# Optimization experiments

Hardware: AMD Instinct MI355X
Metric: run time of the kernel (lower is better)

## Reference

```python
import jax, jax.numpy as jnp
import numpy as np

N = 30000      # nodes
E = 480000     # edges (before self loops)
DIN = 128      # dim_in
DH = 32        # dim_h (per-head out channels)
H1 = 8         # gat1 heads
H2 = 2         # gat2 heads
G = 64         # num graphs in batch
DOUT = 10      # dim_out
NEG_SLOPE = 0.2


def _glorot(key, shape):
    fan_in = shape[0]
    return jax.random.normal(key, shape, dtype=jnp.float32) / np.sqrt(fan_in)


def setup_inputs() -> dict:
    key = jax.random.key(0)
    ks = jax.random.split(key, 16)
    x = jax.random.normal(ks[0], (N, DIN), dtype=jnp.float32)
    edge_index = jax.random.randint(ks[1], (2, E), 0, N, dtype=jnp.int32)
    batch = jnp.sort(jax.random.randint(ks[2], (N,), 0, G, dtype=jnp.int32))
    # GATv2Conv layer 1: lin_l, lin_r (dim_in -> H1*DH), att (H1, DH), bias (H1*DH)
    W1l = _glorot(ks[3], (DIN, H1 * DH))
    W1r = _glorot(ks[4], (DIN, H1 * DH))
    a1 = _glorot(ks[5], (DH, H1)).T  # [H1, DH]
    b1 = jnp.zeros((H1 * DH,), dtype=jnp.float32)
    # GATv2Conv layer 2: (H1*DH -> H2*DH)
    W2l = _glorot(ks[6], (H1 * DH, H2 * DH))
    W2r = _glorot(ks[7], (H1 * DH, H2 * DH))
    a2 = _glorot(ks[8], (DH, H2)).T  # [H2, DH]
    b2 = jnp.zeros((H2 * DH,), dtype=jnp.float32)
    # MLP head: fc1(2*DH -> DH), fc2(DH -> DH//2), fc(DH//2 -> DOUT); stored [in,out]
    fc1_w = _glorot(ks[9], (2 * DH, DH)); fc1_b = jnp.zeros((DH,), jnp.float32)
    fc2_w = _glorot(ks[10], (DH, DH // 2)); fc2_b = jnp.zeros((DH // 2,), jnp.float32)
    fc_w = _glorot(ks[11], (DH // 2, DOUT)); fc_b = jnp.zeros((DOUT,), jnp.float32)
    return {"x": x, "edge_index": edge_index, "batch": batch,
            "W1l": W1l, "W1r": W1r, "a1": a1, "b1": b1,
            "W2l": W2l, "W2r": W2r, "a2": a2, "b2": b2,
            "fc1_w": fc1_w, "fc1_b": fc1_b, "fc2_w": fc2_w, "fc2_b": fc2_b,
            "fc_w": fc_w, "fc_b": fc_b}


def gatv2_conv(x, edge_index, Wl, Wr, att, bias, heads, dh, n):
    """PyG GATv2Conv: concat=True, add_self_loops=True, negative_slope=0.2."""
    src, dst = edge_index[0], edge_index[1]
    loop = jnp.arange(n, dtype=src.dtype)        # self loops (PyG default)
    src = jnp.concatenate([src, loop])
    dst = jnp.concatenate([dst, loop])
    xl = (x @ Wl).reshape(n, heads, dh)          # source transform
    xr = (x @ Wr).reshape(n, heads, dh)          # destination transform
    xj = xl[src]                                  # [Etot, H, dh] message features
    s = jax.nn.leaky_relu(xj + xr[dst], NEG_SLOPE)
    e = jnp.einsum('ehd,hd->eh', s, att)          # per-edge per-head score
    # segment softmax over incoming edges of each destination node
    m = jax.ops.segment_max(e, dst, num_segments=n)
    p = jnp.exp(e - m[dst])
    z = jax.ops.segment_sum(p, dst, num_segments=n)
    alpha = p / z[dst]                            # [Etot, H]
    out = jax.ops.segment_sum(xj * alpha[..., None], dst, num_segments=n)
    return out.reshape(n, heads * dh) + bias


def reference(x, edge_index, batch, W1l, W1r, a1, b1, W2l, W2r, a2, b2,
              fc1_w, fc1_b, fc2_w, fc2_b, fc_w, fc_b):
    h = gatv2_conv(x, edge_index, W1l, W1r, a1, b1, H1, DH, N)
    h = jax.nn.elu(h)
    h = gatv2_conv(h, edge_index, W2l, W2r, a2, b2, H2, DH, N)  # [N, 2*DH]
    # global_mean_pool
    sums = jax.ops.segment_sum(h, batch, num_segments=G)
    cnt = jax.ops.segment_sum(jnp.ones((N,), h.dtype), batch, num_segments=G)
    hg = sums / jnp.maximum(cnt, 1.0)[:, None]    # [G, 2*DH]
    x1 = jax.nn.relu(hg @ fc1_w + fc1_b)
    # dropout p=0.2 is identity in eval mode
    x2 = jax.nn.relu(x1 @ fc2_w + fc2_b)
    c = x2 @ fc_w + fc_b
    return (c, x2)
```

## Files before the change

### kernel.cpp

```cpp
#include <hip/hip_runtime.h>
#include <math.h>

#define DIN 128
#define DH  32
#define H1  8
#define H2  2
#define GNUM 64
#define DOUT 10
#define NEG_SLOPE 0.2f
#define SCAN_B 512

typedef __attribute__((ext_vector_type(8))) short sv8;
typedef __attribute__((ext_vector_type(4))) short sv4;
typedef __attribute__((ext_vector_type(4))) float fv4;

static __device__ __forceinline__ unsigned short f2bf(float f) {
    unsigned int u = __float_as_uint(f);
    unsigned int r = (u + 0x7fffu + ((u >> 16) & 1u)) >> 16;
    return (unsigned short)r;
}
static __device__ __forceinline__ float bf2f(unsigned short h) {
    return __uint_as_float(((unsigned int)h) << 16);
}

__global__ void k_prep(const float* __restrict__ x,
                       const float* __restrict__ W1l, const float* __restrict__ W1r,
                       const float* __restrict__ W2l, const float* __restrict__ W2r,
                       short* __restrict__ B1th, short* __restrict__ B1tl,
                       short* __restrict__ B2th, short* __restrict__ B2tl,
                       unsigned short* __restrict__ Xh, unsigned short* __restrict__ Xl,
                       int* __restrict__ zbase, int nz, int NK) {
    int id = blockIdx.x * blockDim.x + threadIdx.x;
    if (id < nz) zbase[id] = 0;
    const int T1 = 512 * 128;
    const int T2 = 128 * 256;
    if (id < T1) {
        int n = id / 128, k = id - n * 128;
        float v = (n < 256) ? W1l[(size_t)k * 256 + n] : W1r[(size_t)k * 256 + (n - 256)];
        unsigned short h = f2bf(v);
        B1th[id] = (short)h;
        B1tl[id] = (short)f2bf(v - bf2f(h));
    } else if (id < T1 + T2) {
        int id2 = id - T1;
        int n = id2 / 256, k = id2 - n * 256;
        float v = (n < 64) ? W2l[(size_t)k * 64 + n] : W2r[(size_t)k * 64 + (n - 64)];
        unsigned short h = f2bf(v);
        B2th[id2] = (short)h;
        B2tl[id2] = (short)f2bf(v - bf2f(h));
    } else if (id < T1 + T2 + NK) {
        int e = id - T1 - T2;
        float v = x[e];
        unsigned short h = f2bf(v);
        Xh[e] = h;
        Xl[e] = f2bf(v - bf2f(h));
    }
}

__global__ void k_deg(const int* __restrict__ dst, int* __restrict__ deg, int E, int n) {
    int i = blockIdx.x * blockDim.x + threadIdx.x;
    if (i < E) {
        atomicAdd(&deg[dst[i]], 1);
    } else if (i < E + n) {
        atomicAdd(&deg[i - E], 1);
    }
}

__global__ __launch_bounds__(SCAN_B)
void k_scan_partial(const int* __restrict__ deg, int* __restrict__ bsum, int n) {
    int i = blockIdx.x * SCAN_B + threadIdx.x;
    int v = (i < n) ? deg[i] : 0;
    #pragma unroll
    for (int m = 32; m >= 1; m >>= 1) v += __shfl_xor(v, m);
    __shared__ int red[SCAN_B / 64];
    if ((threadIdx.x & 63) == 0) red[threadIdx.x >> 6] = v;
    __syncthreads();
    if (threadIdx.x == 0) {
        int s = 0;
        #pragma unroll
        for (int k = 0; k < SCAN_B / 64; ++k) s += red[k];
        bsum[blockIdx.x] = s;
    }
}

__global__ __launch_bounds__(SCAN_B)
void k_scan_apply(int* __restrict__ deg, int* __restrict__ cursor,
                  const int* __restrict__ bsum, int n, int nb) {
    __shared__ int buf[SCAN_B];
    __shared__ int pfx_s, tot_s;
    const int t = threadIdx.x, b = blockIdx.x;
    if (t < 64) {
        int v = (t < nb) ? bsum[t] : 0;
        int incl = v;
        #pragma unroll
        for (int o = 1; o < 64; o <<= 1) {
            int w = __shfl_up(incl, o);
            if (t >= o) incl += w;
        }
        int pfx = (b == 0) ? 0 : __shfl(incl, b - 1);
        int tot = __shfl(incl, nb - 1);
        if (t == 0) { pfx_s = pfx; tot_s = tot; }
    }
    int i = b * SCAN_B + t;
    int v = (i < n) ? deg[i] : 0;
    buf[t] = v;
    __syncthreads();
    for (int o = 1; o < SCAN_B; o <<= 1) {
        int a = (t >= o) ? buf[t - o] : 0;
        __syncthreads();
        buf[t] += a;
        __syncthreads();
    }
    int excl = buf[t] - v + pfx_s;
    if (i < n) { deg[i] = excl; cursor[i] = excl; }
    if (b == 0 && t == 0) deg[n] = tot_s;
}

__global__ void k_scatter(const int* __restrict__ src, const int* __restrict__ dst,
                          int* __restrict__ cursor, int* __restrict__ csr_src, int E, int n) {
    int i = blockIdx.x * blockDim.x + threadIdx.x;
    if (i < E) {
        int d = dst[i];
        int pos = atomicAdd(&cursor[d], 1);
        csr_src[pos] = src[i];
    } else if (i < E + n) {
        int v = i - E;
        int pos = atomicAdd(&cursor[v], 1);
        csr_src[pos] = v;
    }
}

__global__ __launch_bounds__(256)
void k_gemm_split(const unsigned short* __restrict__ Ah, const unsigned short* __restrict__ Al,
                  const short* __restrict__ Bth, const short* __restrict__ Btl,
                  unsigned short* __restrict__ Cl, float* __restrict__ Cr,
                  int M, int K, int Ntot, int NL) {
    __shared__ union {
        struct { short hi[128 * 40]; short lo[128 * 40]; } a;
        float c[64 * 132];
    } sm;
    const int tid = threadIdx.x;
    const int lane = tid & 63;
    const int wid = tid >> 6;
    const int wm = wid & 1, wn = wid >> 1;
    const int m0 = blockIdx.x * 128;
    const int n0 = blockIdx.y * 128;
    const int l15 = lane & 15, q = lane >> 4;

    fv4 acc[4][4] = {};

    for (int kk = 0; kk < K; kk += 32) {
        __syncthreads();
        #pragma unroll
        for (int i = 0; i < 4; ++i) {
            int idx = tid + i * 256;
            int arr = idx >> 9;
            int c = idx & 511;
            int row = c >> 2, qq = c & 3;
            int mg = m0 + row;
            const unsigned short* srcp = arr ? Al : Ah;
            sv8 v = { 0, 0, 0, 0, 0, 0, 0, 0 };
            if (mg < M) v = *(const sv8*)(srcp + (size_t)mg * K + kk + qq * 8);
            short* dst = arr ? sm.a.lo : sm.a.hi;
            *(sv8*)&dst[row * 40 + qq * 8] = v;
        }
        __syncthreads();

        sv8 bh[4], bl[4];
        #pragma unroll
        for (int fn = 0; fn < 4; ++fn) {
            int ng = n0 + wn * 64 + fn * 16 + l15;
            bh[fn] = *(const sv8*)(Bth + (size_t)ng * K + kk + q * 8);
            bl[fn] = *(const sv8*)(Btl + (size_t)ng * K + kk + q * 8);
        }
        #pragma unroll
        for (int fm = 0; fm < 4; ++fm) {
            int rl = wm * 64 + fm * 16 + l15;
            sv8 ah = *(const sv8*)&sm.a.hi[rl * 40 + q * 8];
            sv8 al = *(const sv8*)&sm.a.lo[rl * 40 + q * 8];
            #pragma unroll
            for (int fn = 0; fn < 4; ++fn) {
                acc[fm][fn] = __builtin_amdgcn_mfma_f32_16x16x32_bf16(ah, bh[fn], acc[fm][fn], 0, 0, 0);
                acc[fm][fn] = __builtin_amdgcn_mfma_f32_16x16x32_bf16(ah, bl[fn], acc[fm][fn], 0, 0, 0);
                acc[fm][fn] = __builtin_amdgcn_mfma_f32_16x16x32_bf16(al, bh[fn], acc[fm][fn], 0, 0, 0);
            }
        }
    }

    const int NR = Ntot - NL;
    #pragma unroll
    for (int s = 0; s < 2; ++s) {
        __syncthreads();
        if (wm == s) {
            #pragma unroll
            for (int fm = 0; fm < 4; ++fm)
                #pragma unroll
                for (int fn = 0; fn < 4; ++fn)
                    #pragma unroll
                    for (int r = 0; r < 4; ++r)
                        sm.c[(fm * 16 + q * 4 + r) * 132 + wn * 64 + fn * 16 + l15] = acc[fm][fn][r];
        }
        __syncthreads();
        #pragma unroll
        for (int i = 0; i < 2; ++i) {
            int lr = (tid >> 3) + i * 32;
            int grow = m0 + s * 64 + lr;
            if (grow < M) {
                #pragma unroll
                for (int k4 = 0; k4 < 4; ++k4) {
                    int jj = (tid & 7) + k4 * 8;
                    float4 vv = *(float4*)&sm.c[lr * 132 + jj * 4];
                    int gcol = n0 + jj * 4;
                    if (gcol < NL) {
                        ushort4 uu;
                        uu.x = f2bf(vv.x); uu.y = f2bf(vv.y);
                        uu.z = f2bf(vv.z); uu.w = f2bf(vv.w);
                        *(ushort4*)(Cl + (size_t)grow * NL + gcol) = uu;
                    } else {
                        *(float4*)(Cr + (size_t)grow * NR + (gcol - NL)) = vv;
                    }
                }
            }
        }
    }
}

__global__ __launch_bounds__(256)
void k_gemm_bf(const unsigned short* __restrict__ A, const short* __restrict__ Bth,
               const short* __restrict__ Btl,
               unsigned short* __restrict__ Cl, float* __restrict__ Cr,
               int M, int K, int Ntot, int NL) {
    __shared__ union {
        short a[128 * 40];
        float c[64 * 132];
    } sm;
    const int tid = threadIdx.x;
    const int lane = tid & 63;
    const int wid = tid >> 6;
    const int wm = wid & 1, wn = wid >> 1;
    const int m0 = blockIdx.x * 128;
    const int n0 = blockIdx.y * 128;
    const int l15 = lane & 15, q = lane >> 4;

    fv4 acc[4][4] = {};

    for (int kk = 0; kk < K; kk += 32) {
        __syncthreads();
        #pragma unroll
        for (int i = 0; i < 2; ++i) {
            int idx = tid + i * 256;
            int row = idx >> 2, qq = idx & 3;
            int mg = m0 + row;
            sv8 v = { 0, 0, 0, 0, 0, 0, 0, 0 };
            if (mg < M) v = *(const sv8*)(A + (size_t)mg * K + kk + qq * 8);
            *(sv8*)&sm.a[row * 40 + qq * 8] = v;
        }
        __syncthreads();

        sv8 bh[4], bl[4];
        #pragma unroll
        for (int fn = 0; fn < 4; ++fn) {
            int ng = n0 + wn * 64 + fn * 16 + l15;
            bh[fn] = *(const sv8*)(Bth + (size_t)ng * K + kk + q * 8);
            bl[fn] = *(const sv8*)(Btl + (size_t)ng * K + kk + q * 8);
        }
        #pragma unroll
        for (int fm = 0; fm < 4; ++fm) {
            int rl = wm * 64 + fm * 16 + l15;
            sv8 ah = *(const sv8*)&sm.a[rl * 40 + q * 8];
            #pragma unroll
            for (int fn = 0; fn < 4; ++fn) {
                acc[fm][fn] = __builtin_amdgcn_mfma_f32_16x16x32_bf16(ah, bh[fn], acc[fm][fn], 0, 0, 0);
                acc[fm][fn] = __builtin_amdgcn_mfma_f32_16x16x32_bf16(ah, bl[fn], acc[fm][fn], 0, 0, 0);
            }
        }
    }

    const int NR = Ntot - NL;
    #pragma unroll
    for (int s = 0; s < 2; ++s) {
        __syncthreads();
        if (wm == s) {
            #pragma unroll
            for (int fm = 0; fm < 4; ++fm)
                #pragma unroll
                for (int fn = 0; fn < 4; ++fn)
                    #pragma unroll
                    for (int r = 0; r < 4; ++r)
                        sm.c[(fm * 16 + q * 4 + r) * 132 + wn * 64 + fn * 16 + l15] = acc[fm][fn][r];
        }
        __syncthreads();
        #pragma unroll
        for (int i = 0; i < 2; ++i) {
            int lr = (tid >> 3) + i * 32;
            int grow = m0 + s * 64 + lr;
            if (grow < M) {
                #pragma unroll
                for (int k4 = 0; k4 < 4; ++k4) {
                    int jj = (tid & 7) + k4 * 8;
                    float4 vv = *(float4*)&sm.c[lr * 132 + jj * 4];
                    int gcol = n0 + jj * 4;
                    if (gcol < NL) {
                        ushort4 uu;
                        uu.x = f2bf(vv.x); uu.y = f2bf(vv.y);
                        uu.z = f2bf(vv.z); uu.w = f2bf(vv.w);
                        *(ushort4*)(Cl + (size_t)grow * NL + gcol) = uu;
                    } else {
                        *(float4*)(Cr + (size_t)grow * NR + (gcol - NL)) = vv;
                    }
                }
            }
        }
    }
}

__global__ __launch_bounds__(64)
void k_edge1(const unsigned short* __restrict__ XLB, const float* __restrict__ XR,
             const int* __restrict__ offs, const int* __restrict__ csr,
             const float* __restrict__ att, const float* __restrict__ bias,
             unsigned short* __restrict__ out, int n) {
    const int lane = threadIdx.x;
    const int v = blockIdx.x;
    const int li = lane & 31;
    const int half = lane >> 5;
    float av[8], xr[8];
    #pragma unroll
    for (int k = 0; k < 8; ++k) av[k] = att[li * 8 + k];
    #pragma unroll
    for (int k = 0; k < 8; ++k) xr[k] = XR[(size_t)v * 256 + li * 8 + k];
    const uint4* XL4 = (const uint4*)XLB;
    float z = 0.f;
    float acc[8] = {};
    const int e0 = offs[v], e1 = offs[v + 1];
    for (int j0 = e0; j0 < e1; j0 += 4) {
        #pragma unroll
        for (int p = 0; p < 2; ++p) {
            int j = j0 + p * 2 + half;
            bool valid = (j < e1);
            int jj = valid ? j : (e1 - 1);
            int src = csr[jj];
            uint4 u = XL4[(size_t)src * 32 + li];
            float f[8];
            f[0] = __uint_as_float(u.x << 16);  f[1] = __uint_as_float(u.x & 0xffff0000u);
            f[2] = __uint_as_float(u.y << 16);  f[3] = __uint_as_float(u.y & 0xffff0000u);
            f[4] = __uint_as_float(u.z << 16);  f[5] = __uint_as_float(u.z & 0xffff0000u);
            f[6] = __uint_as_float(u.w << 16);  f[7] = __uint_as_float(u.w & 0xffff0000u);
            float s1 = 0.f, s2 = 0.f;
            #pragma unroll
            for (int k = 0; k < 8; ++k) {
                float t = f[k] + xr[k];
                s1 = fmaf(t, av[k], s1);
                s2 = fmaf(fabsf(t), av[k], s2);
            }
            float s = fmaf(0.6f, s1, 0.4f * s2);
            s += __shfl_xor(s, 1);
            s += __shfl_xor(s, 2);
            float w = valid ? __expf(s) : 0.f;
            z += w;
            #pragma unroll
            for (int k = 0; k < 8; ++k) acc[k] = fmaf(w, f[k], acc[k]);
        }
    }
    z += __shfl_xor(z, 32);
    #pragma unroll
    for (int k = 0; k < 8; ++k) acc[k] += __shfl_xor(acc[k], 32);
    if (half == 0) {
        const float rz = 1.f / z;
        unsigned int o[4];
        #pragma unroll
        for (int k2 = 0; k2 < 4; ++k2) {
            float lo = fmaf(acc[k2 * 2 + 0], rz, bias[li * 8 + k2 * 2 + 0]);
            float hi = fmaf(acc[k2 * 2 + 1], rz, bias[li * 8 + k2 * 2 + 1]);
            lo = (lo > 0.f) ? lo : (__expf(lo) - 1.f);
            hi = (hi > 0.f) ? hi : (__expf(hi) - 1.f);
            o[k2] = (unsigned int)f2bf(lo) | ((unsigned int)f2bf(hi) << 16);
        }
        uint4 ov = { o[0], o[1], o[2], o[3] };
        *(uint4*)(out + (size_t)v * 256 + li * 8) = ov;
    }
}

__global__ __launch_bounds__(64)
void k_edge2(const unsigned short* __restrict__ XLB, const float* __restrict__ XR,
             const int* __restrict__ offs, const int* __restrict__ csr,
             const float* __restrict__ att, const float* __restrict__ bias,
             float* __restrict__ out, int n) {
    const int lane = threadIdx.x;
    const int v = blockIdx.x;
    const int li = lane & 7;
    const int slot = lane >> 3;
    float av[8], xr[8];
    #pragma unroll
    for (int k = 0; k < 8; ++k) av[k] = att[li * 8 + k];
    #pragma unroll
    for (int k = 0; k < 8; ++k) xr[k] = XR[(size_t)v * 64 + li * 8 + k];
    const uint4* XL4 = (const uint4*)XLB;
    float z = 0.f;
    float acc[8] = {};
    const int e0 = offs[v], e1 = offs[v + 1];
    for (int j0 = e0; j0 < e1; j0 += 8) {
        int j = j0 + slot;
        bool valid = (j < e1);
        int jj = valid ? j : (e1 - 1);
        int src = csr[jj];
        uint4 u = XL4[(size_t)src * 8 + li];
        float f[8];
        f[0] = __uint_as_float(u.x << 16);  f[1] = __uint_as_float(u.x & 0xffff0000u);
        f[2] = __uint_as_float(u.y << 16);  f[3] = __uint_as_float(u.y & 0xffff0000u);
        f[4] = __uint_as_float(u.z << 16);  f[5] = __uint_as_float(u.z & 0xffff0000u);
        f[6] = __uint_as_float(u.w << 16);  f[7] = __uint_as_float(u.w & 0xffff0000u);
        float s1 = 0.f, s2 = 0.f;
        #pragma unroll
        for (int k = 0; k < 8; ++k) {
            float t = f[k] + xr[k];
            s1 = fmaf(t, av[k], s1);
            s2 = fmaf(fabsf(t), av[k], s2);
        }
        float s = fmaf(0.6f, s1, 0.4f * s2);
        s += __shfl_xor(s, 1);
        s += __shfl_xor(s, 2);
        float w = valid ? __expf(s) : 0.f;
        z += w;
        #pragma unroll
        for (int k = 0; k < 8; ++k) acc[k] = fmaf(w, f[k], acc[k]);
    }
    z += __shfl_xor(z, 8);  z += __shfl_xor(z, 16);  z += __shfl_xor(z, 32);
    #pragma unroll
    for (int k = 0; k < 8; ++k) {
        acc[k] += __shfl_xor(acc[k], 8);
        acc[k] += __shfl_xor(acc[k], 16);
        acc[k] += __shfl_xor(acc[k], 32);
    }
    if (slot == 0) {
        const float rz = 1.f / z;
        float o[8];
        #pragma unroll
        for (int k = 0; k < 8; ++k)
            o[k] = fmaf(acc[k], rz, bias[li * 8 + k]);
        float4 o0 = { o[0], o[1], o[2], o[3] };
        float4 o1 = { o[4], o[5], o[6], o[7] };
        *(float4*)(out + (size_t)v * 64 + li * 8 + 0) = o0;
        *(float4*)(out + (size_t)v * 64 + li * 8 + 4) = o1;
    }
}

__global__ __launch_bounds__(256)
void k_pool_mlp(const float* __restrict__ out2, const int* __restrict__ batch,
                const float* __restrict__ fc1w, const float* __restrict__ fc1b,
                const float* __restrict__ fc2w, const float* __restrict__ fc2b,
                const float* __restrict__ fcw,  const float* __restrict__ fcb,
                float* __restrict__ outc, float* __restrict__ outx2, int n) {
    const int g = blockIdx.x;
    const int t = threadIdx.x;
    const int lane = t & 63;
    const int w = t >> 6;
    __shared__ float red[4][64];
    __shared__ float hg_s[64];
    __shared__ float x1_s[32];
    __shared__ float x2_s[16];

    int lo = 0, hi = n;
    while (lo < hi) { int mid = (lo + hi) >> 1; if (batch[mid] < g) lo = mid + 1; else hi = mid; }
    const int start = lo;
    hi = n;
    while (lo < hi) { int mid = (lo + hi) >> 1; if (batch[mid] < g + 1) lo = mid + 1; else hi = mid; }
    const int end = lo;

    float s = 0.f;
    for (int v = start + w; v < end; v += 4)
        s += out2[(size_t)v * 64 + lane];
    red[w][lane] = s;
    __syncthreads();
    if (w == 0) {
        float tot = red[0][lane] + red[1][lane] + red[2][lane] + red[3][lane];
        float cnt = fmaxf((float)(end - start), 1.0f);
        hg_s[lane] = tot / cnt;
    }
    __syncthreads();
    if (t < 32) {
        float a = fc1b[t];
        #pragma unroll
        for (int k = 0; k < 64; ++k) a = fmaf(hg_s[k], fc1w[k * 32 + t], a);
        x1_s[t] = fmaxf(a, 0.f);
    }
    __syncthreads();
    if (t < 16) {
        float a = fc2b[t];
        #pragma unroll
        for (int k = 0; k < 32; ++k) a = fmaf(x1_s[k], fc2w[k * 16 + t], a);
        x2_s[t] = fmaxf(a, 0.f);
    }
    __syncthreads();
    if (t < DOUT) {
        float a = fcb[t];
        #pragma unroll
        for (int k = 0; k < 16; ++k) a = fmaf(x2_s[k], fcw[k * 10 + t], a);
        outc[g * DOUT + t] = a;
    }
    if (t < 16) outx2[g * 16 + t] = x2_s[t];
}

extern "C" void kernel_launch(void* const* d_in, const int* in_sizes, int n_in,
                              void* d_out, int out_size, void* d_ws, size_t ws_size,
                              hipStream_t stream) {
    const float* x    = (const float*)d_in[0];
    const int*   ei   = (const int*)d_in[1];
    const int*   batch= (const int*)d_in[2];
    const float* W1l  = (const float*)d_in[3];
    const float* W1r  = (const float*)d_in[4];
    const float* a1   = (const float*)d_in[5];
    const float* b1   = (const float*)d_in[6];
    const float* W2l  = (const float*)d_in[7];
    const float* W2r  = (const float*)d_in[8];
    const float* a2   = (const float*)d_in[9];
    const float* b2   = (const float*)d_in[10];
    const float* fc1w = (const float*)d_in[11];
    const float* fc1b = (const float*)d_in[12];
    const float* fc2w = (const float*)d_in[13];
    const float* fc2b = (const float*)d_in[14];
    const float* fcw  = (const float*)d_in[15];
    const float* fcb  = (const float*)d_in[16];

    const int N = in_sizes[2];
    const int E = in_sizes[1] / 2;
    const int ET = E + N;
    const int* esrc = ei;
    const int* edst = ei + E;
    const int NB = (N + SCAN_B - 1) / SCAN_B;

    char* ws = (char*)d_ws;
    size_t off = 0;
    unsigned short* xl1b = (unsigned short*)(ws + off);  off += (size_t)N * 256 * 2;
    float* xr1  = (float*)(ws + off);            off += (size_t)N * 256 * 4;
    unsigned short* h1b = (unsigned short*)(ws + off);   off += (size_t)N * 256 * 2;
    int*   deg   = (int*)(ws + off);             off += ((size_t)(N + 1) * 4 + 255) & ~255ull;
    int*   cursor= (int*)(ws + off);             off += ((size_t)N * 4 + 255) & ~255ull;
    int*   csr   = (int*)(ws + off);             off += ((size_t)ET * 4 + 255) & ~255ull;
    int*   bsum  = (int*)(ws + off);             off += ((size_t)(NB + 1) * 4 + 255) & ~255ull;
    short* B1th  = (short*)(ws + off);           off += (size_t)512 * 128 * 2;
    short* B1tl  = (short*)(ws + off);           off += (size_t)512 * 128 * 2;
    short* B2th  = (short*)(ws + off);           off += (size_t)128 * 256 * 2;
    short* B2tl  = (short*)(ws + off);           off += (size_t)128 * 256 * 2;
    unsigned short* Xh = (unsigned short*)(ws + off);    off += (size_t)N * 128 * 2;
    unsigned short* Xl = (unsigned short*)(ws + off);    off += (size_t)N * 128 * 2;
    unsigned short* xl2b = xl1b;
    float* xr2  = xr1;
    float* out2 = xr1 + (size_t)N * 64;
    (void)ws_size; (void)n_in; (void)out_size;

    float* outc  = (float*)d_out;
    float* outx2 = (float*)d_out + GNUM * DOUT;

    const int prep_tot = 512 * 128 + 128 * 256 + N * 128;
    k_prep<<<(prep_tot + 255) / 256, 256, 0, stream>>>(
        x, W1l, W1r, W2l, W2r, B1th, B1tl, B2th, B2tl, Xh, Xl, deg, N + 1, N * 128);

    int tb = 256;
    int gb = (ET + tb - 1) / tb;
    k_deg<<<gb, tb, 0, stream>>>(edst, deg, E, N);
    k_scan_partial<<<NB, SCAN_B, 0, stream>>>(deg, bsum, N);
    k_scan_apply<<<NB, SCAN_B, 0, stream>>>(deg, cursor, bsum, N, NB);
    k_scatter<<<gb, tb, 0, stream>>>(esrc, edst, cursor, csr, E, N);

    dim3 g1((N + 127) / 128, 4);
    k_gemm_split<<<g1, 256, 0, stream>>>(Xh, Xl, B1th, B1tl, xl1b, xr1, N, DIN, 512, 256);

    k_edge1<<<N, 64, 0, stream>>>(xl1b, xr1, deg, csr, a1, b1, h1b, N);

    dim3 g2((N + 127) / 128, 1);
    k_gemm_bf<<<g2, 256, 0, stream>>>(h1b, B2th, B2tl, xl2b, xr2, N, 256, 128, 64);

    k_edge2<<<N, 64, 0, stream>>>(xl2b, xr2, deg, csr, a2, b2, out2, N);

    k_pool_mlp<<<GNUM, 256, 0, stream>>>(out2, batch, fc1w, fc1b, fc2w, fc2b,
                                         fcw, fcb, outc, outx2, N);
}
```

Before: 303.1 us.

## Fuse x bf16 hi/lo split into layer-1 GEMM and widen N tile

The separate pass in k_prep that split x into bf16 hi/lo arrays is removed. The layer-1 GEMM now reads fp32 x directly and does the split while staging A into shared memory, which avoids writing and re-reading two N×128 bf16 buffers. The N tile per block also doubles from 128 to 256, so A is loaded and converted half as many times. The cost is twice the accumulator registers (acc[4][8]), which may lower occupancy, and a longer epilogue with more barriers.

```diff
diff --git a/kernel.cpp b/kernel.cpp
--- a/kernel.cpp
+++ b/kernel.cpp
@@ -23,13 +23,11 @@
     return __uint_as_float(((unsigned int)h) << 16);
 }
 
-__global__ void k_prep(const float* __restrict__ x,
-                       const float* __restrict__ W1l, const float* __restrict__ W1r,
+__global__ void k_prep(const float* __restrict__ W1l, const float* __restrict__ W1r,
                        const float* __restrict__ W2l, const float* __restrict__ W2r,
                        short* __restrict__ B1th, short* __restrict__ B1tl,
                        short* __restrict__ B2th, short* __restrict__ B2tl,
-                       unsigned short* __restrict__ Xh, unsigned short* __restrict__ Xl,
-                       int* __restrict__ zbase, int nz, int NK) {
+                       int* __restrict__ zbase, int nz) {
     int id = blockIdx.x * blockDim.x + threadIdx.x;
     if (id < nz) zbase[id] = 0;
     const int T1 = 512 * 128;
@@ -47,12 +45,6 @@
         unsigned short h = f2bf(v);
         B2th[id2] = (short)h;
         B2tl[id2] = (short)f2bf(v - bf2f(h));
-    } else if (id < T1 + T2 + NK) {
-        int e = id - T1 - T2;
-        float v = x[e];
-        unsigned short h = f2bf(v);
-        Xh[e] = h;
-        Xl[e] = f2bf(v - bf2f(h));
     }
 }
 
@@ -130,10 +122,10 @@
 }
 
 __global__ __launch_bounds__(256)
-void k_gemm_split(const unsigned short* __restrict__ Ah, const unsigned short* __restrict__ Al,
-                  const short* __restrict__ Bth, const short* __restrict__ Btl,
-                  unsigned short* __restrict__ Cl, float* __restrict__ Cr,
-                  int M, int K, int Ntot, int NL) {
+void k_gemm1(const float* __restrict__ A,
+             const short* __restrict__ Bth, const short* __restrict__ Btl,
+             unsigned short* __restrict__ Cl, float* __restrict__ Cr,
+             int M, int K, int Ntot, int NL) {
     __shared__ union {
         struct { short hi[128 * 40]; short lo[128 * 40]; } a;
         float c[64 * 132];
@@ -143,32 +135,34 @@
     const int wid = tid >> 6;
     const int wm = wid & 1, wn = wid >> 1;
     const int m0 = blockIdx.x * 128;
-    const int n0 = blockIdx.y * 128;
+    const int n0 = blockIdx.y * 256;
     const int l15 = lane & 15, q = lane >> 4;
 
-    fv4 acc[4][4] = {};
+    fv4 acc[4][8] = {};
 
     for (int kk = 0; kk < K; kk += 32) {
         __syncthreads();
         #pragma unroll
         for (int i = 0; i < 4; ++i) {
             int idx = tid + i * 256;
-            int arr = idx >> 9;
-            int c = idx & 511;
-            int row = c >> 2, qq = c & 3;
-            int mg = m0 + row;
-            const unsigned short* srcp = arr ? Al : Ah;
-            sv8 v = { 0, 0, 0, 0, 0, 0, 0, 0 };
-            if (mg < M) v = *(const sv8*)(srcp + (size_t)mg * K + kk + qq * 8);
-            short* dst = arr ? sm.a.lo : sm.a.hi;
-            *(sv8*)&dst[row * 40 + qq * 8] = v;
-        }
-        __syncthreads();
-
-        sv8 bh[4], bl[4];
-        #pragma unroll
-        for (int fn = 0; fn < 4; ++fn) {
-            int ng = n0 + wn * 64 + fn * 16 + l15;
+            int row = idx >> 3;
+            int qq  = idx & 7;
+            int mg  = m0 + row;
+            float4 v = make_float4(0.f, 0.f, 0.f, 0.f);
+            if (mg < M) v = *(const float4*)(A + (size_t)mg * K + kk + qq * 4);
+            unsigned short hx = f2bf(v.x), hy = f2bf(v.y), hz = f2bf(v.z), hw = f2bf(v.w);
+            sv4 hi = { (short)hx, (short)hy, (short)hz, (short)hw };
+            sv4 lo = { (short)f2bf(v.x - bf2f(hx)), (short)f2bf(v.y - bf2f(hy)),
+                       (short)f2bf(v.z - bf2f(hz)), (short)f2bf(v.w - bf2f(hw)) };
+            *(sv4*)&sm.a.hi[row * 40 + qq * 4] = hi;
+            *(sv4*)&sm.a.lo[row * 40 + qq * 4] = lo;
+        }
+        __syncthreads();
+
+        sv8 bh[8], bl[8];
+        #pragma unroll
+        for (int fn = 0; fn < 8; ++fn) {
+            int ng = n0 + wn * 128 + fn * 16 + l15;
             bh[fn] = *(const sv8*)(Bth + (size_t)ng * K + kk + q * 8);
             bl[fn] = *(const sv8*)(Btl + (size_t)ng * K + kk + q * 8);
         }
@@ -178,7 +172,7 @@
             sv8 ah = *(const sv8*)&sm.a.hi[rl * 40 + q * 8];
             sv8 al = *(const sv8*)&sm.a.lo[rl * 40 + q * 8];
             #pragma unroll
-            for (int fn = 0; fn < 4; ++fn) {
+            for (int fn = 0; fn < 8; ++fn) {
                 acc[fm][fn] = __builtin_amdgcn_mfma_f32_16x16x32_bf16(ah, bh[fn], acc[fm][fn], 0, 0, 0);
                 acc[fm][fn] = __builtin_amdgcn_mfma_f32_16x16x32_bf16(ah, bl[fn], acc[fm][fn], 0, 0, 0);
                 acc[fm][fn] = __builtin_amdgcn_mfma_f32_16x16x32_bf16(al, bh[fn], acc[fm][fn], 0, 0, 0);
@@ -189,34 +183,37 @@
     const int NR = Ntot - NL;
     #pragma unroll
     for (int s = 0; s < 2; ++s) {
-        __syncthreads();
-        if (wm == s) {
+        #pragma unroll
+        for (int cn = 0; cn < 2; ++cn) {
+            __syncthreads();
+            if (wm == s && wn == cn) {
+                #pragma unroll
+                for (int fm = 0; fm < 4; ++fm)
+                    #pragma unroll
+                    for (int fn = 0; fn < 8; ++fn)
+                        #pragma unroll
+                        for (int r = 0; r < 4; ++r)
+                            sm.c[(fm * 16 + q * 4 + r) * 132 + fn * 16 + l15] = acc[fm][fn][r];
+            }
+            __syncthreads();
             #pragma unroll
-            for (int fm = 0; fm < 4; ++fm)
-                #pragma unroll
-                for (int fn = 0; fn < 4; ++fn)
+            for (int i = 0; i < 2; ++i) {
+                int lr = (tid >> 3) + i * 32;
+                int grow = m0 + s * 64 + lr;
+                if (grow < M) {
                     #pragma unroll
-                    for (int r = 0; r < 4; ++r)
-                        sm.c[(fm * 16 + q * 4 + r) * 132 + wn * 64 + fn * 16 + l15] = acc[fm][fn][r];
-        }
-        __syncthreads();
-        #pragma unroll
-        for (int i = 0; i < 2; ++i) {
-            int lr = (tid >> 3) + i * 32;
-            int grow = m0 + s * 64 + lr;
-            if (grow < M) {
-                #pragma unroll
-                for (int k4 = 0; k4 < 4; ++k4) {
-                    int jj = (tid & 7) + k4 * 8;
-                    float4 vv = *(float4*)&sm.c[lr * 132 + jj * 4];
-                    int gcol = n0 + jj * 4;
-                    if (gcol < NL) {
-                        ushort4 uu;
-                        uu.x = f2bf(vv.x); uu.y = f2bf(vv.y);
-                        uu.z = f2bf(vv.z); uu.w = f2bf(vv.w);
-                        *(ushort4*)(Cl + (size_t)grow * NL + gcol) = uu;
-                    } else {
-                        *(float4*)(Cr + (size_t)grow * NR + (gcol - NL)) = vv;
+                    for (int k4 = 0; k4 < 4; ++k4) {
+                        int jj = (tid & 7) + k4 * 8;
+                        float4 vv = *(float4*)&sm.c[lr * 132 + jj * 4];
+                        int gcol = n0 + cn * 128 + jj * 4;
+                        if (gcol < NL) {
+                            ushort4 uu;
+                            uu.x = f2bf(vv.x); uu.y = f2bf(vv.y);
+                            uu.z = f2bf(vv.z); uu.w = f2bf(vv.w);
+                            *(ushort4*)(Cl + (size_t)grow * NL + gcol) = uu;
+                        } else {
+                            *(float4*)(Cr + (size_t)grow * NR + (gcol - NL)) = vv;
+                        }
                     }
                 }
             }
@@ -540,8 +537,6 @@
     short* B1tl  = (short*)(ws + off);           off += (size_t)512 * 128 * 2;
     short* B2th  = (short*)(ws + off);           off += (size_t)128 * 256 * 2;
     short* B2tl  = (short*)(ws + off);           off += (size_t)128 * 256 * 2;
-    unsigned short* Xh = (unsigned short*)(ws + off);    off += (size_t)N * 128 * 2;
-    unsigned short* Xl = (unsigned short*)(ws + off);    off += (size_t)N * 128 * 2;
     unsigned short* xl2b = xl1b;
     float* xr2  = xr1;
     float* out2 = xr1 + (size_t)N * 64;
@@ -550,9 +545,9 @@
     float* outc  = (float*)d_out;
     float* outx2 = (float*)d_out + GNUM * DOUT;
 
-    const int prep_tot = 512 * 128 + 128 * 256 + N * 128;
+    const int prep_tot = 512 * 128 + 128 * 256;
     k_prep<<<(prep_tot + 255) / 256, 256, 0, stream>>>(
-        x, W1l, W1r, W2l, W2r, B1th, B1tl, B2th, B2tl, Xh, Xl, deg, N + 1, N * 128);
+        W1l, W1r, W2l, W2r, B1th, B1tl, B2th, B2tl, deg, N + 1);
 
     int tb = 256;
     int gb = (ET + tb - 1) / tb;
@@ -561,8 +556,8 @@
     k_scan_apply<<<NB, SCAN_B, 0, stream>>>(deg, cursor, bsum, N, NB);
     k_scatter<<<gb, tb, 0, stream>>>(esrc, edst, cursor, csr, E, N);
 
-    dim3 g1((N + 127) / 128, 4);
-    k_gemm_split<<<g1, 256, 0, stream>>>(Xh, Xl, B1th, B1tl, xl1b, xr1, N, DIN, 512, 256);
+    dim3 g1((N + 127) / 128, 2);
+    k_gemm1<<<g1, 256, 0, stream>>>(x, B1th, B1tl, xl1b, xr1, N, DIN, 512, 256);
 
     k_edge1<<<N, 64, 0, stream>>>(xl1b, xr1, deg, csr, a1, b1, h1b, N);
 
```

Measured after the change: 304.3 us. About the same (+0.4%).
